# Performance work log

Measured on AMD Instinct MI355X. Metric: run time of the kernel, lower is better.

The kernel has to match this reference:

```python
import jax, jax.numpy as jnp
import numpy as np

EPS = 1e-5      # BatchNorm eps (torch default)
SLOPE = 0.2     # LeakyReLU negative slope


def _ico_conv(x, neigh, W, b):
    """Spherical 1-ring conv: gather K=7 neighbors per vertex, then linear.
    x: (B, C, V) float; neigh: (V, K) int; W: (O, C*K); b: (O,) -> (B, O, V).
    """
    B, C, V = x.shape
    K = neigh.shape[1]
    g = x[:, :, neigh]                             # (B, C, V, K) gather
    g = g.transpose(0, 2, 1, 3).reshape(B, V, C * K)  # per-vertex patch, C-major
    return jnp.einsum('bvi,oi->bov', g, W) + b[None, :, None]


def _bn_lrelu(x, gamma, beta):
    """BatchNorm1d (batch stats only, track_running_stats=False) + LeakyReLU(0.2).
    x: (B, C, V); normalize each channel over (B, V) with biased variance.
    """
    mean = x.mean(axis=(0, 2), keepdims=True)
    var = x.var(axis=(0, 2), keepdims=True)
    y = (x - mean) * jax.lax.rsqrt(var + EPS)
    y = y * gamma[None, :, None] + beta[None, :, None]
    return jnp.where(y >= 0, y, SLOPE * y)


def setup_inputs() -> dict:
    key = jax.random.key(0)
    ks = jax.random.split(key, 8)
    B, IN_CH, OUT_CH = 16, 32, 64
    N_FINE, N_COARSE, K = 163842, 40962, 7   # ico order 7 -> order 6
    x = jax.random.normal(ks[0], (B, IN_CH, N_FINE), dtype=jnp.float32)
    down_neigh_indices = jax.random.randint(ks[1], (N_COARSE, K), 0, N_FINE)
    conv_neigh_indices = jax.random.randint(ks[2], (N_COARSE, K), 0, N_COARSE)
    s1 = 1.0 / np.sqrt(IN_CH * K)
    s2 = 1.0 / np.sqrt(OUT_CH * K)
    w1 = jax.random.uniform(ks[3], (OUT_CH, IN_CH * K), minval=-s1, maxval=s1, dtype=jnp.float32)
    b1 = jax.random.uniform(ks[4], (OUT_CH,), minval=-s1, maxval=s1, dtype=jnp.float32)
    w2 = jax.random.uniform(ks[5], (OUT_CH, OUT_CH * K), minval=-s2, maxval=s2, dtype=jnp.float32)
    b2 = jax.random.uniform(ks[6], (OUT_CH,), minval=-s2, maxval=s2, dtype=jnp.float32)
    g1 = jnp.ones((OUT_CH,), jnp.float32)
    beta1 = jnp.zeros((OUT_CH,), jnp.float32)
    g2 = jnp.ones((OUT_CH,), jnp.float32)
    beta2 = jnp.zeros((OUT_CH,), jnp.float32)
    return dict(x=x, w1=w1, b1=b1, g1=g1, beta1=beta1, w2=w2, b2=b2, g2=g2,
                beta2=beta2, conv_neigh_indices=conv_neigh_indices,
                down_neigh_indices=down_neigh_indices)


def reference(x, w1, b1, g1, beta1, w2, b2, g2, beta2,
              conv_neigh_indices, down_neigh_indices):
    # IcoPoolLayer, mean mode: gather 7 fine-mesh neighbors per coarse vertex,
    # average over the neighborhood. (B, C, N_fine) -> (B, C, N_coarse)
    xp = x[:, :, down_neigh_indices].mean(axis=-1)
    # (conv -> BN -> LeakyReLU) x 2 at the coarse sampling
    h = _bn_lrelu(_ico_conv(xp, conv_neigh_indices, w1, b1), g1, beta1)
    h = _bn_lrelu(_ico_conv(h, conv_neigh_indices, w2, b2), g2, beta2)
    return h  # max_pool_indices is None for mean pooling
```

## Files before the change

### kernel.cpp

```cpp
#include <hip/hip_runtime.h>
#include <hip/hip_bf16.h>


#define B_SZ     16
#define CIN      32
#define CMID     64
#define VFINE    163842
#define VC       40962
#define KNB      7

typedef __attribute__((ext_vector_type(8))) short  short8;
typedef __attribute__((ext_vector_type(4))) float  f32x4;
typedef __attribute__((ext_vector_type(4))) unsigned short u16x4;
typedef __attribute__((ext_vector_type(2))) unsigned short u16x2;

__device__ inline float bf2f(unsigned short u) {
    return __builtin_bit_cast(float, (unsigned int)(((unsigned int)u) << 16));
}
__device__ inline unsigned short f2bf(float f) {
    __hip_bfloat16 h = __float2bfloat16(f);
    return __builtin_bit_cast(unsigned short, h);
}

__global__ void prep_w(const float* __restrict__ w1, const float* __restrict__ w2,
                       unsigned short* __restrict__ w1f, unsigned short* __restrict__ w2f) {
    int tid = blockIdx.x * blockDim.x + threadIdx.x;
    int stride = gridDim.x * blockDim.x;
    const int total1 = 7 * 4 * 64 * 8;
    for (int idx = tid; idx < total1; idx += stride) {
        int j = idx & 7, l = (idx >> 3) & 63, t = (idx >> 9) & 3, cc = idx >> 11;
        int o = t * 16 + (l & 15);
        int kk = (l >> 4) * 8 + j;
        w1f[idx] = f2bf(w1[o * 224 + kk * 7 + cc]);
    }
    const int total2 = 14 * 4 * 64 * 8;
    for (int idx = tid; idx < total2; idx += stride) {
        int j = idx & 7, l = (idx >> 3) & 63, t = (idx >> 9) & 3, cc = idx >> 11;
        int o = t * 16 + (l & 15);
        int kk = (l >> 4) * 8 + j;
        int k = cc >> 1, ch = cc & 1;
        int c = ch * 32 + kk;
        w2f[idx] = f2bf(w2[o * 448 + c * 7 + k]);
    }
}

__global__ __launch_bounds__(256) void transpose_x(const float* __restrict__ x,
                                                   unsigned short* __restrict__ xt, int vf) {
    __shared__ __align__(16) unsigned short lds[256 * 64];
    const int t = threadIdx.x;
    const int v0 = blockIdx.x * 64;
    const int j  = t & 15;
    const int r0 = t >> 4;
    const int lane = t & 63;
    const int wv = (t >> 6) * 16;

#pragma unroll
    for (int p = 0; p < 2; ++p) {
        if (p) __syncthreads();
#pragma unroll
        for (int it = 0; it < 16; ++it) {
            int r = r0 + it * 16;
            int row = p * 256 + r;
            int vg = v0 + 4 * j;
            f32x4 d = {0.f, 0.f, 0.f, 0.f};
            if (vg + 3 < vf) {
                d = *reinterpret_cast<const f32x4*>(x + (size_t)row * vf + vg);
            } else {
#pragma unroll
                for (int q = 0; q < 4; ++q)
                    if (vg + q < vf) d[q] = x[(size_t)row * vf + vg + q];
            }
            int jswz = j ^ ((r >> 2) & 15);
            u16x4 s;
#pragma unroll
            for (int q = 0; q < 4; ++q) s[q] = f2bf(d[q]);
            *reinterpret_cast<u16x4*>(lds + r * 64 + jswz * 4) = s;
        }
        __syncthreads();
#pragma unroll
        for (int pr = 0; pr < 8; ++pr) {
            int v = wv + pr * 2 + (lane >> 5);
#pragma unroll
            for (int half = 0; half < 2; ++half) {
                int g = (lane & 31) + 32 * half;
                u16x4 o;
#pragma unroll
                for (int q = 0; q < 4; ++q) {
                    int r = 4 * g + q;
                    int jswz = (v >> 2) ^ ((r >> 2) & 15);
                    o[q] = lds[r * 64 + jswz * 4 + (v & 3)];
                }
                if (v0 + v < vf)
                    *reinterpret_cast<u16x4*>(xt + (size_t)(v0 + v) * 512 + p * 256 + 4 * g) = o;
            }
        }
    }
}

__global__ __launch_bounds__(256) void pool_k(const unsigned short* __restrict__ xt,
                                              const int* __restrict__ dn,
                                              unsigned short* __restrict__ xp, int vc) {
    int wid = (blockIdx.x * blockDim.x + threadIdx.x) >> 6;
    int lane = threadIdx.x & 63;
    if (wid >= vc) return;
    float acc[8];
#pragma unroll
    for (int j = 0; j < 8; ++j) acc[j] = 0.f;
#pragma unroll
    for (int k = 0; k < 7; ++k) {
        int n = dn[(size_t)wid * 7 + k];
        short8 d = *reinterpret_cast<const short8*>(xt + (size_t)n * 512 + lane * 8);
#pragma unroll
        for (int j = 0; j < 8; ++j) acc[j] += bf2f((unsigned short)d[j]);
    }
    short8 o;
#pragma unroll
    for (int j = 0; j < 8; ++j) o[j] = (short)f2bf(acc[j] * (1.f / 7.f));
    *reinterpret_cast<short8*>(xp + (size_t)wid * 512 + lane * 8) = o;
}

template <int CCH>
__global__ __launch_bounds__(256) void conv_mfma(const unsigned short* __restrict__ xin,
                                                 const int* __restrict__ neigh,
                                                 const unsigned short* __restrict__ wfrag,
                                                 unsigned short* __restrict__ hout,
                                                 float* __restrict__ stats,
                                                 int vc, int ngroups) {
    constexpr int C = 32 * CCH;
    constexpr int NCHUNK = 7 * CCH;
    __shared__ __align__(16) unsigned short wlds[NCHUNK * 4 * 64 * 8];
    __shared__ float bsum[128];
    for (int i = threadIdx.x; i < NCHUNK * 256; i += 256)
        reinterpret_cast<short8*>(wlds)[i] = reinterpret_cast<const short8*>(wfrag)[i];
    if (threadIdx.x < 128) bsum[threadIdx.x] = 0.f;
    __syncthreads();

    const int wid = threadIdx.x >> 6;
    const int lane = threadIdx.x & 63;
    const int lb = lane & 15, lg = lane >> 4;

    float ssum[16], ssq[16];
#pragma unroll
    for (int i = 0; i < 16; ++i) { ssum[i] = 0.f; ssq[i] = 0.f; }

    for (int grp = blockIdx.x; grp < ngroups; grp += gridDim.x) {
        const int v0 = grp * 16 + wid * 4;
        f32x4 acc[4][4];
#pragma unroll
        for (int i = 0; i < 4; ++i)
#pragma unroll
            for (int t = 0; t < 4; ++t) acc[i][t] = (f32x4){0.f, 0.f, 0.f, 0.f};

#pragma unroll 1
        for (int k = 0; k < 7; ++k) {
            int n[4];
#pragma unroll
            for (int i = 0; i < 4; ++i) {
                int v = v0 + i;
                n[i] = (v < vc) ? neigh[(size_t)v * 7 + k] : 0;
            }
#pragma unroll
            for (int ch = 0; ch < CCH; ++ch) {
                const int chunk = k * CCH + ch;
                const short8* wp = reinterpret_cast<const short8*>(wlds) + (chunk * 4) * 64 + lane;
                short8 a0 = wp[0];
                short8 a1 = wp[64];
                short8 a2 = wp[128];
                short8 a3 = wp[192];
#pragma unroll
                for (int i = 0; i < 4; ++i) {
                    const short8 b = *reinterpret_cast<const short8*>(
                        xin + (size_t)n[i] * (16 * C) + lb * C + ch * 32 + lg * 8);
                    acc[i][0] = __builtin_amdgcn_mfma_f32_16x16x32_bf16(a0, b, acc[i][0], 0, 0, 0);
                    acc[i][1] = __builtin_amdgcn_mfma_f32_16x16x32_bf16(a1, b, acc[i][1], 0, 0, 0);
                    acc[i][2] = __builtin_amdgcn_mfma_f32_16x16x32_bf16(a2, b, acc[i][2], 0, 0, 0);
                    acc[i][3] = __builtin_amdgcn_mfma_f32_16x16x32_bf16(a3, b, acc[i][3], 0, 0, 0);
                }
            }
        }
#pragma unroll
        for (int i = 0; i < 4; ++i) {
            const int v = v0 + i;
            if (v < vc) {
#pragma unroll
                for (int t = 0; t < 4; ++t) {
                    u16x4 st;
#pragma unroll
                    for (int r = 0; r < 4; ++r) {
                        float f = acc[i][t][r];
                        ssum[t * 4 + r] += f;
                        ssq[t * 4 + r] += f * f;
                        st[r] = f2bf(f);
                    }
                    *reinterpret_cast<u16x4*>(hout + (size_t)v * 1024 + lb * 64 + t * 16 + lg * 4) = st;
                }
            }
        }
    }
#pragma unroll
    for (int m = 1; m <= 8; m <<= 1) {
#pragma unroll
        for (int i = 0; i < 16; ++i) {
            ssum[i] += __shfl_xor(ssum[i], m, 64);
            ssq[i] += __shfl_xor(ssq[i], m, 64);
        }
    }
    if (lb == 0) {
#pragma unroll
        for (int t = 0; t < 4; ++t)
#pragma unroll
            for (int r = 0; r < 4; ++r) {
                int o = t * 16 + lg * 4 + r;
                atomicAdd(&bsum[o], ssum[t * 4 + r]);
                atomicAdd(&bsum[64 + o], ssq[t * 4 + r]);
            }
    }
    __syncthreads();
    if (threadIdx.x < 128) atomicAdd(&stats[threadIdx.x], bsum[threadIdx.x]);
}

__global__ void bn_params(const float* __restrict__ stats, const float* __restrict__ gamma,
                          const float* __restrict__ beta, float* __restrict__ params, float inv_n) {
    int o = threadIdx.x;
    if (o < 64) {
        float mean = stats[o] * inv_n;
        float var = stats[64 + o] * inv_n - mean * mean;
        float sc = gamma[o] * rsqrtf(var + 1e-5f);
        params[o] = sc;
        params[64 + o] = beta[o] - mean * sc;
    }
}

__global__ __launch_bounds__(256) void bn_apply(unsigned short* __restrict__ h,
                                                const float* __restrict__ params, int total8) {
    int stride = gridDim.x * blockDim.x;
    int idx0 = blockIdx.x * blockDim.x + threadIdx.x;
    int c0 = (idx0 & 7) * 8;
    float sc[8], sh[8];
#pragma unroll
    for (int j = 0; j < 8; ++j) { sc[j] = params[c0 + j]; sh[j] = params[64 + c0 + j]; }
    for (int idx = idx0; idx < total8; idx += stride) {
        short8 d = *reinterpret_cast<const short8*>(h + (size_t)idx * 8);
        short8 o;
#pragma unroll
        for (int j = 0; j < 8; ++j) {
            float y = sc[j] * bf2f((unsigned short)d[j]) + sh[j];
            y = fmaxf(y, 0.2f * y);
            o[j] = (short)f2bf(y);
        }
        *reinterpret_cast<short8*>(h + (size_t)idx * 8) = o;
    }
}

__global__ __launch_bounds__(256) void final_out(const unsigned short* __restrict__ h2,
                                                 const float* __restrict__ params,
                                                 float* __restrict__ out, int vc) {
    __shared__ float lds[128 * 65];
    const int t = threadIdx.x;
    const int v0 = blockIdx.x * 64;
    const int sub = t & 15, vloc = t >> 4;
    const int o0 = (sub & 7) * 8;
    float sc[8], sh[8];
#pragma unroll
    for (int j = 0; j < 8; ++j) { sc[j] = params[o0 + j]; sh[j] = params[64 + o0 + j]; }
    for (int c = 0; c < 8; ++c) {
        if (c) __syncthreads();
#pragma unroll
        for (int i = 0; i < 4; ++i) {
            int v = v0 + vloc + 16 * i;
            short8 d = {0, 0, 0, 0, 0, 0, 0, 0};
            if (v < vc)
                d = *reinterpret_cast<const short8*>(h2 + (size_t)v * 1024 + c * 128 + sub * 8);
#pragma unroll
            for (int j = 0; j < 8; ++j) {
                float y = sc[j] * bf2f((unsigned short)d[j]) + sh[j];
                y = fmaxf(y, 0.2f * y);
                lds[(sub * 8 + j) * 65 + vloc + 16 * i] = y;
            }
        }
        __syncthreads();
        for (int q = 0; q < 32; ++q) {
            int idx = t + 256 * q;
            int r = idx >> 6, vv = idx & 63;
            if (v0 + vv < vc)
                out[(size_t)(c * 128 + r) * vc + v0 + vv] = lds[r * 65 + vv];
        }
    }
}

extern "C" void kernel_launch(void* const* d_in, const int* in_sizes, int n_in,
                              void* d_out, int out_size, void* d_ws, size_t ws_size,
                              hipStream_t stream) {
    const float* x   = (const float*)d_in[0];
    const float* w1  = (const float*)d_in[1];
    const float* g1  = (const float*)d_in[3];
    const float* be1 = (const float*)d_in[4];
    const float* w2  = (const float*)d_in[5];
    const float* g2  = (const float*)d_in[7];
    const float* be2 = (const float*)d_in[8];
    const int* cn    = (const int*)d_in[9];
    const int* dn    = (const int*)d_in[10];
    float* out = (float*)d_out;

    char* ws = (char*)d_ws;
    size_t off = 0;
    auto take = [&](size_t bytes) { size_t o = off; off = (off + bytes + 255) & ~(size_t)255; return o; };
    unsigned short* xp  = (unsigned short*)(ws + take((size_t)VC * 512 * 2));
    unsigned short* h1  = (unsigned short*)(ws + take((size_t)VC * 1024 * 2));
    unsigned short* h2  = (unsigned short*)(ws + take((size_t)VC * 1024 * 2));
    unsigned short* w1f = (unsigned short*)(ws + take(7 * 4 * 64 * 8 * 2));
    unsigned short* w2f = (unsigned short*)(ws + take(14 * 4 * 64 * 8 * 2));
    float* stats        = (float*)(ws + take(256 * 4));
    float* params       = (float*)(ws + take(256 * 4));

    unsigned short* xt = (unsigned short*)d_out;

    const float inv_n = 1.0f / (16.0f * (float)VC);
    const int ngroups = (VC + 15) / 16;

    hipMemsetAsync(stats, 0, 256 * 4, stream);
    prep_w<<<32, 256, 0, stream>>>(w1, w2, w1f, w2f);
    transpose_x<<<(VFINE + 63) / 64, 256, 0, stream>>>(x, xt, VFINE);
    pool_k<<<(VC + 3) / 4, 256, 0, stream>>>(xt, dn, xp, VC);
    conv_mfma<1><<<512, 256, 0, stream>>>(xp, cn, w1f, h1, stats, VC, ngroups);
    bn_params<<<1, 64, 0, stream>>>(stats, g1, be1, params, inv_n);
    bn_apply<<<2048, 256, 0, stream>>>(h1, params, VC * 1024 / 8);
    conv_mfma<2><<<512, 256, 0, stream>>>(h1, cn, w2f, h2, stats + 128, VC, ngroups);
    bn_params<<<1, 64, 0, stream>>>(stats + 128, g2, be2, params + 128, inv_n);
    final_out<<<(VC + 63) / 64, 256, 0, stream>>>(h2, params + 128, out, VC);
}
```

Measured before the change: 514.1 us.

## Fuse BN1 apply into conv2 gather, fold memset, rework transpose and output stores

Drops the standalone bn_apply pass and applies BN1 scale/shift plus LeakyReLU to each gathered neighbor fragment inside the second conv, before the MFMA. This removes one full read-write pass over h1. The catch is that every vertex now gets normalized about seven times, once per neighbor that gathers it. The stats memset moves into prep_w to save a launch. transpose_x switches to a padded LDS layout that gives a simpler vector read-out, and final_out writes float4 vectors instead of scalars.

```diff
diff --git a/kernel.cpp b/kernel.cpp
--- a/kernel.cpp
+++ b/kernel.cpp
@@ -12,7 +12,6 @@
 typedef __attribute__((ext_vector_type(8))) short  short8;
 typedef __attribute__((ext_vector_type(4))) float  f32x4;
 typedef __attribute__((ext_vector_type(4))) unsigned short u16x4;
-typedef __attribute__((ext_vector_type(2))) unsigned short u16x2;
 
 __device__ inline float bf2f(unsigned short u) {
     return __builtin_bit_cast(float, (unsigned int)(((unsigned int)u) << 16));
@@ -23,9 +22,11 @@
 }
 
 __global__ void prep_w(const float* __restrict__ w1, const float* __restrict__ w2,
-                       unsigned short* __restrict__ w1f, unsigned short* __restrict__ w2f) {
+                       unsigned short* __restrict__ w1f, unsigned short* __restrict__ w2f,
+                       float* __restrict__ stats) {
     int tid = blockIdx.x * blockDim.x + threadIdx.x;
     int stride = gridDim.x * blockDim.x;
+    if (blockIdx.x == 0 && threadIdx.x < 256) stats[threadIdx.x] = 0.f;
     const int total1 = 7 * 4 * 64 * 8;
     for (int idx = tid; idx < total1; idx += stride) {
         int j = idx & 7, l = (idx >> 3) & 63, t = (idx >> 9) & 3, cc = idx >> 11;
@@ -46,13 +47,13 @@
 
 __global__ __launch_bounds__(256) void transpose_x(const float* __restrict__ x,
                                                    unsigned short* __restrict__ xt, int vf) {
-    __shared__ __align__(16) unsigned short lds[256 * 64];
+    __shared__ __align__(16) unsigned short lds[64 * 258];
     const int t = threadIdx.x;
     const int v0 = blockIdx.x * 64;
     const int j  = t & 15;
     const int r0 = t >> 4;
     const int lane = t & 63;
-    const int wv = (t >> 6) * 16;
+    const int wid = t >> 6;
 
 #pragma unroll
     for (int p = 0; p < 2; ++p) {
@@ -70,29 +71,17 @@
                 for (int q = 0; q < 4; ++q)
                     if (vg + q < vf) d[q] = x[(size_t)row * vf + vg + q];
             }
-            int jswz = j ^ ((r >> 2) & 15);
-            u16x4 s;
-#pragma unroll
-            for (int q = 0; q < 4; ++q) s[q] = f2bf(d[q]);
-            *reinterpret_cast<u16x4*>(lds + r * 64 + jswz * 4) = s;
+#pragma unroll
+            for (int q = 0; q < 4; ++q)
+                lds[(4 * j + q) * 258 + r] = f2bf(d[q]);
         }
         __syncthreads();
 #pragma unroll
-        for (int pr = 0; pr < 8; ++pr) {
-            int v = wv + pr * 2 + (lane >> 5);
-#pragma unroll
-            for (int half = 0; half < 2; ++half) {
-                int g = (lane & 31) + 32 * half;
-                u16x4 o;
-#pragma unroll
-                for (int q = 0; q < 4; ++q) {
-                    int r = 4 * g + q;
-                    int jswz = (v >> 2) ^ ((r >> 2) & 15);
-                    o[q] = lds[r * 64 + jswz * 4 + (v & 3)];
-                }
-                if (v0 + v < vf)
-                    *reinterpret_cast<u16x4*>(xt + (size_t)(v0 + v) * 512 + p * 256 + 4 * g) = o;
-            }
+        for (int i = 0; i < 16; ++i) {
+            int v = wid * 16 + i;
+            u16x4 o = *reinterpret_cast<const u16x4*>(lds + v * 258 + 4 * lane);
+            if (v0 + v < vf)
+                *reinterpret_cast<u16x4*>(xt + (size_t)(v0 + v) * 512 + p * 256 + 4 * lane) = o;
         }
     }
 }
@@ -119,10 +108,11 @@
     *reinterpret_cast<short8*>(xp + (size_t)wid * 512 + lane * 8) = o;
 }
 
-template <int CCH>
+template <int CCH, bool BN_IN>
 __global__ __launch_bounds__(256) void conv_mfma(const unsigned short* __restrict__ xin,
                                                  const int* __restrict__ neigh,
                                                  const unsigned short* __restrict__ wfrag,
+                                                 const float* __restrict__ bnp,
                                                  unsigned short* __restrict__ hout,
                                                  float* __restrict__ stats,
                                                  int vc, int ngroups) {
@@ -139,6 +129,17 @@
     const int lane = threadIdx.x & 63;
     const int lb = lane & 15, lg = lane >> 4;
 
+    float scv[CCH][8], shv[CCH][8];
+    if constexpr (BN_IN) {
+#pragma unroll
+        for (int ch = 0; ch < CCH; ++ch)
+#pragma unroll
+            for (int j = 0; j < 8; ++j) {
+                scv[ch][j] = bnp[ch * 32 + lg * 8 + j];
+                shv[ch][j] = bnp[64 + ch * 32 + lg * 8 + j];
+            }
+    }
+
     float ssum[16], ssq[16];
 #pragma unroll
     for (int i = 0; i < 16; ++i) { ssum[i] = 0.f; ssq[i] = 0.f; }
@@ -151,8 +152,7 @@
 #pragma unroll
             for (int t = 0; t < 4; ++t) acc[i][t] = (f32x4){0.f, 0.f, 0.f, 0.f};
 
-#pragma unroll 1
-        for (int k = 0; k < 7; ++k) {
+        auto do_k = [&](int k) {
             int n[4];
 #pragma unroll
             for (int i = 0; i < 4; ++i) {
@@ -169,15 +169,33 @@
                 short8 a3 = wp[192];
 #pragma unroll
                 for (int i = 0; i < 4; ++i) {
-                    const short8 b = *reinterpret_cast<const short8*>(
+                    short8 b = *reinterpret_cast<const short8*>(
                         xin + (size_t)n[i] * (16 * C) + lb * C + ch * 32 + lg * 8);
+                    if constexpr (BN_IN) {
+                        short8 bb;
+#pragma unroll
+                        for (int j = 0; j < 8; ++j) {
+                            float z = fmaf(scv[ch][j], bf2f((unsigned short)b[j]), shv[ch][j]);
+                            z = fmaxf(z, 0.2f * z);
+                            bb[j] = (short)f2bf(z);
+                        }
+                        b = bb;
+                    }
                     acc[i][0] = __builtin_amdgcn_mfma_f32_16x16x32_bf16(a0, b, acc[i][0], 0, 0, 0);
                     acc[i][1] = __builtin_amdgcn_mfma_f32_16x16x32_bf16(a1, b, acc[i][1], 0, 0, 0);
                     acc[i][2] = __builtin_amdgcn_mfma_f32_16x16x32_bf16(a2, b, acc[i][2], 0, 0, 0);
                     acc[i][3] = __builtin_amdgcn_mfma_f32_16x16x32_bf16(a3, b, acc[i][3], 0, 0, 0);
                 }
             }
-        }
+        };
+        if constexpr (BN_IN) {
+#pragma unroll 2
+            for (int k = 0; k < 7; ++k) do_k(k);
+        } else {
+#pragma unroll 1
+            for (int k = 0; k < 7; ++k) do_k(k);
+        }
+
 #pragma unroll
         for (int i = 0; i < 4; ++i) {
             const int v = v0 + i;
@@ -231,27 +249,6 @@
     }
 }
 
-__global__ __launch_bounds__(256) void bn_apply(unsigned short* __restrict__ h,
-                                                const float* __restrict__ params, int total8) {
-    int stride = gridDim.x * blockDim.x;
-    int idx0 = blockIdx.x * blockDim.x + threadIdx.x;
-    int c0 = (idx0 & 7) * 8;
-    float sc[8], sh[8];
-#pragma unroll
-    for (int j = 0; j < 8; ++j) { sc[j] = params[c0 + j]; sh[j] = params[64 + c0 + j]; }
-    for (int idx = idx0; idx < total8; idx += stride) {
-        short8 d = *reinterpret_cast<const short8*>(h + (size_t)idx * 8);
-        short8 o;
-#pragma unroll
-        for (int j = 0; j < 8; ++j) {
-            float y = sc[j] * bf2f((unsigned short)d[j]) + sh[j];
-            y = fmaxf(y, 0.2f * y);
-            o[j] = (short)f2bf(y);
-        }
-        *reinterpret_cast<short8*>(h + (size_t)idx * 8) = o;
-    }
-}
-
 __global__ __launch_bounds__(256) void final_out(const unsigned short* __restrict__ h2,
                                                  const float* __restrict__ params,
                                                  float* __restrict__ out, int vc) {
@@ -279,11 +276,21 @@
             }
         }
         __syncthreads();
-        for (int q = 0; q < 32; ++q) {
+#pragma unroll
+        for (int q = 0; q < 8; ++q) {
             int idx = t + 256 * q;
-            int r = idx >> 6, vv = idx & 63;
-            if (v0 + vv < vc)
-                out[(size_t)(c * 128 + r) * vc + v0 + vv] = lds[r * 65 + vv];
+            int r = idx >> 4;
+            int vq = (idx & 15) * 4;
+            int v = v0 + vq;
+            const float* lp = lds + r * 65 + vq;
+            if (v + 3 < vc) {
+                f32x4 o = {lp[0], lp[1], lp[2], lp[3]};
+                *reinterpret_cast<f32x4*>(out + (size_t)(c * 128 + r) * vc + v) = o;
+            } else {
+#pragma unroll
+                for (int e = 0; e < 4; ++e)
+                    if (v + e < vc) out[(size_t)(c * 128 + r) * vc + v + e] = lp[e];
+            }
         }
     }
 }
@@ -318,14 +325,12 @@
     const float inv_n = 1.0f / (16.0f * (float)VC);
     const int ngroups = (VC + 15) / 16;
 
-    hipMemsetAsync(stats, 0, 256 * 4, stream);
-    prep_w<<<32, 256, 0, stream>>>(w1, w2, w1f, w2f);
+    prep_w<<<32, 256, 0, stream>>>(w1, w2, w1f, w2f, stats);
     transpose_x<<<(VFINE + 63) / 64, 256, 0, stream>>>(x, xt, VFINE);
     pool_k<<<(VC + 3) / 4, 256, 0, stream>>>(xt, dn, xp, VC);
-    conv_mfma<1><<<512, 256, 0, stream>>>(xp, cn, w1f, h1, stats, VC, ngroups);
+    conv_mfma<1, false><<<512, 256, 0, stream>>>(xp, cn, w1f, nullptr, h1, stats, VC, ngroups);
     bn_params<<<1, 64, 0, stream>>>(stats, g1, be1, params, inv_n);
-    bn_apply<<<2048, 256, 0, stream>>>(h1, params, VC * 1024 / 8);
-    conv_mfma<2><<<512, 256, 0, stream>>>(h1, cn, w2f, h2, stats + 128, VC, ngroups);
+    conv_mfma<2, true><<<512, 256, 0, stream>>>(h1, cn, w2f, params, h2, stats + 128, VC, ngroups);
     bn_params<<<1, 64, 0, stream>>>(stats + 128, g2, be2, params + 128, inv_n);
     final_out<<<(VC + 63) / 64, 256, 0, stream>>>(h2, params + 128, out, VC);
 }
```

After: 587.6 us. +14.3%, slower.
